# Kernel optimization log

Measured on AMD Instinct MI355X. Metric: run time of the kernel, lower is better.

## Reference

```python
import jax, jax.numpy as jnp
import numpy as np

N = 8192          # rays
S = 128           # steps per ray (cfg.n_steps_fixed)
POS_BANDS = 10    # positional-encoding bands for positions
VD_BANDS = 4      # bands for view directions (default in _encode_viewdir)
EARLY_STOP_T = 1e-4


def pos_enc(x, num_bands):
    """[..., 3] -> [..., 3 + 2*3*num_bands], interleaved [x, sin(f*x), cos(f*x), ...]."""
    parts = [x]
    for i in range(num_bands):  # small fixed loop over frequency bands
        f = jnp.asarray(2.0 ** i, dtype=x.dtype)
        parts.append(jnp.sin(f * x))
        parts.append(jnp.cos(f * x))
    return jnp.concatenate(parts, axis=-1)


def setup_inputs() -> dict:
    key = jax.random.key(0)
    ks = jax.random.split(key, 10)
    orig = 0.1 * jax.random.normal(ks[0], (N, 3), jnp.float32)
    dirs = jax.random.normal(ks[1], (N, 3), jnp.float32)
    dirs = dirs / (jnp.linalg.norm(dirs, axis=-1, keepdims=True) + 1e-8)
    tmin = 0.5 + 0.5 * jax.random.uniform(ks[2], (N,), jnp.float32)
    tmax = tmin + 1.0 + jax.random.uniform(ks[3], (N,), jnp.float32)
    d_enc = 3 + 2 * 3 * POS_BANDS          # 63
    d_vd = 3 + 2 * 3 * VD_BANDS            # 27
    hid, feat = 64, 15
    W1 = jax.random.normal(ks[4], (d_enc, hid), jnp.float32) / np.sqrt(d_enc)
    b1 = jnp.zeros((hid,), jnp.float32)
    W2 = jax.random.normal(ks[5], (hid, 1 + feat), jnp.float32) / np.sqrt(hid)
    b2 = jnp.zeros((1 + feat,), jnp.float32)
    V1 = jax.random.normal(ks[6], (feat + d_vd, hid), jnp.float32) / np.sqrt(feat + d_vd)
    c1 = jnp.zeros((hid,), jnp.float32)
    V2 = jax.random.normal(ks[7], (hid, 3), jnp.float32) / np.sqrt(hid)
    c2 = jnp.zeros((3,), jnp.float32)
    return {"orig": orig, "dirs": dirs, "tmin": tmin, "tmax": tmax,
            "W1": W1, "b1": b1, "W2": W2, "b2": b2,
            "V1": V1, "c1": c1, "V2": V2, "c2": c2}


def reference(orig, dirs, tmin, tmax, W1, b1, W2, b2, V1, c1, V2, c2):
    # --- fixed-step sampling ---
    t_uniform = jnp.linspace(0.0, 1.0, S, dtype=jnp.float32)          # [S]
    t = tmin[:, None] + t_uniform[None, :] * (tmax - tmin)[:, None]   # [N, S]
    dt = jnp.mean(tmax - tmin) / S                                    # scalar step size

    # --- positions and encoder ---
    pos = orig[:, None, :] + dirs[:, None, :] * t[..., None]          # [N, S, 3]
    enc = pos_enc(pos, POS_BANDS)                                     # [N, S, 63]

    # --- field MLP: sigma + rgb features ---
    h = jax.nn.relu(enc @ W1 + b1)                                    # [N, S, 64]
    out = h @ W2 + b2                                                 # [N, S, 16]
    sigma = jax.nn.relu(out[..., 0])                                  # [N, S]
    rgb_feat = out[..., 1:]                                           # [N, S, 15]

    # --- rgb head with view-direction PE ---
    vd = dirs / (jnp.linalg.norm(dirs, axis=-1, keepdims=True) + 1e-8)
    vd_enc = pos_enc(vd, VD_BANDS)                                    # [N, 27]
    vd_enc = jnp.broadcast_to(vd_enc[:, None, :], (rgb_feat.shape[0], S, vd_enc.shape[-1]))
    rgb_in = jnp.concatenate([rgb_feat, vd_enc], axis=-1)             # [N, S, 42]
    rgb_steps = jax.nn.sigmoid(jax.nn.relu(rgb_in @ V1 + c1) @ V2 + c2)  # [N, S, 3]

    # --- alpha compositing with early stop (dense-masked equivalent) ---
    alpha = 1.0 - jnp.exp(-sigma * dt)                                # [N, S]
    one_minus = 1.0 - alpha
    T_excl = jnp.concatenate(
        [jnp.ones_like(alpha[:, :1]), jnp.cumprod(one_minus, axis=1)[:, :-1]], axis=1
    )                                                                 # transmittance before each step
    active = T_excl > EARLY_STOP_T                                    # ray still marching
    weights = T_excl * alpha * active                                 # [N, S]
    rgb_out = jnp.sum(weights[..., None] * rgb_steps, axis=1)         # [N, 3]
    T_out = jnp.prod(jnp.where(active, one_minus, 1.0), axis=1)       # final transmittance at stop
    return rgb_out, T_out
```

## Files before the change

### kernel.cpp

```cpp
#include <hip/hip_runtime.h>
#include <hip/hip_bf16.h>

#define NRAYS 8192
#define SAMP  128
#define DVD   27
#define NFEAT 15

typedef float  f32x4  __attribute__((ext_vector_type(4)));
typedef short  short8 __attribute__((ext_vector_type(8)));
typedef unsigned int u32x2 __attribute__((ext_vector_type(2)));

static __device__ __forceinline__ void stbf(short* p, float x) {
    union { unsigned u; struct { short lo, hi; } s; } v;
    v.u = __float_as_uint(x) + 0x8000u;
    *p = v.s.hi;
}
static __device__ __forceinline__ float bf2f(short s) {
    return __uint_as_float(((unsigned)(unsigned short)s) << 16);
}
static __device__ __forceinline__ unsigned pk2bf(float lo, float hi) {
    unsigned r;
    asm("v_cvt_pk_bf16_f32 %0, %1, %2" : "=v"(r) : "v"(lo), "v"(hi));
    return r;
}
static __device__ __forceinline__ float sin_fast(float x) {
    float r = x * 0.15915494309189535f;
    r = r - floorf(r);
    return __builtin_amdgcn_sinf(r);
}
static __device__ __forceinline__ float cos_fast(float x) {
    float r = x * 0.15915494309189535f;
    r = r - floorf(r);
    return __builtin_amdgcn_cosf(r);
}

#define SMEM_BYTES 32208

__global__ void __launch_bounds__(256)
march_kernel(const float* __restrict__ orig,
             const float* __restrict__ dirs,
             const float* __restrict__ tmin,
             const float* __restrict__ tmax,
             const float* __restrict__ W1,
             const float* __restrict__ b1,
             const float* __restrict__ W2,
             const float* __restrict__ b2,
             const float* __restrict__ V1,
             const float* __restrict__ c1,
             const float* __restrict__ V2,
             const float* __restrict__ c2,
             float* __restrict__ out) {
    __shared__ __align__(16) char smem[SMEM_BYTES];
    short* const sW1t = (short*)(smem);
    short* const sW2t = (short*)(smem + 9216);
    short* const sV1t = (short*)(smem + 11520);
    short* const sV2t = (short*)(smem + 15616);
    short* const sEa  = (short*)(smem);
    short* const sGa  = (short*)(smem + 18432);
    float* const sOm  = (float*)(smem + 26624);
    short* const sRgb = (short*)(smem + 28672);
    float* const sVde = (float*)(smem + 31744);
    float* const sRed = (float*)(smem + 32192);

    const int tid  = threadIdx.x;
    const int lane = tid & 63;
    const int wave = tid >> 6;
    const int ray  = blockIdx.x * 4 + wave;

    {
        const float4* tm0 = (const float4*)tmin;
        const float4* tm1 = (const float4*)tmax;
        float s = 0.0f;
        #pragma unroll
        for (int it = 0; it < 8; it++) {
            const int i = tid + it * 256;
            const float4 a = tm1[i], b = tm0[i];
            s += (a.x - b.x) + (a.y - b.y) + (a.z - b.z) + (a.w - b.w);
        }
        #pragma unroll
        for (int off = 32; off > 0; off >>= 1)
            s += __shfl_xor(s, off, 64);
        if (lane == 0) sRed[wave] = s;
    }

    for (int i = tid; i < 63 * 64; i += 256) {
        const int k = i >> 6, n = i & 63;
        const int nk = (k < 3) ? (60 + k) : (k - 3);
        stbf(&sW1t[n * 72 + nk], W1[i]);
    }
    for (int i = tid; i < 64; i += 256)
        stbf(&sW1t[i * 72 + 63], b1[i]);
    for (int i = tid; i < 64 * 16; i += 256) {
        const int k = i >> 4, n = i & 15;
        stbf(&sW2t[n * 72 + k], W2[i]);
    }
    for (int i = tid; i < 15 * 64; i += 256) {
        const int k = i >> 6, n = i & 63;
        stbf(&sV1t[n * 32 + k], V1[i]);
    }
    for (int i = tid; i < 64; i += 256)
        stbf(&sV1t[i * 32 + 15], c1[i]);
    for (int i = tid; i < 64 * 16; i += 256) {
        const int n = i >> 4, k = 16 + (i & 15);
        sV1t[n * 32 + k] = 0;
    }
    for (int i = tid; i < 192; i += 256) {
        const int k = i / 3, n = i - 3 * k;
        stbf(&sV2t[n * 72 + k], V2[i]);
    }

    const float ox = orig[ray * 3 + 0];
    const float oy = orig[ray * 3 + 1];
    const float oz = orig[ray * 3 + 2];
    const float dx = dirs[ray * 3 + 0];
    const float dy = dirs[ray * 3 + 1];
    const float dz = dirs[ray * 3 + 2];
    const float t0v = tmin[ray];
    const float trange = tmax[ray] - t0v;

    {
        const float nrm = sqrtf(dx * dx + dy * dy + dz * dz);
        const float inv = 1.0f / (nrm + 1e-8f);
        const float vx = dx * inv, vy = dy * inv, vz = dz * inv;
        if (lane < DVD) {
            float val;
            if (lane < 3) {
                val = (lane == 0) ? vx : ((lane == 1) ? vy : vz);
            } else {
                const int q = lane - 3;
                const int b = q / 6;
                const int r = q - 6 * b;
                const bool isSin = (r < 3);
                const int d = isSin ? r : (r - 3);
                const float comp = (d == 0) ? vx : ((d == 1) ? vy : vz);
                const float a = (float)(1 << b) * comp;
                val = isSin ? sin_fast(a) : cos_fast(a);
            }
            sVde[wave * 28 + lane] = val;
        }
    }
    __syncthreads();

    const float dtv = (sRed[0] + sRed[1] + sRed[2] + sRed[3]) *
                      (1.0f / ((float)NRAYS * (float)SAMP));

    const int nfr  = lane & 15;
    const int quad = lane >> 4;

    short8 w1f[4][2], w2f[2], v1f[4], v2f[2];
    #pragma unroll
    for (int nt = 0; nt < 4; nt++)
        #pragma unroll
        for (int kt = 0; kt < 2; kt++)
            w1f[nt][kt] = *(const short8*)&sW1t[(4 * nfr + nt) * 72 + quad * 8 + kt * 32];
    #pragma unroll
    for (int kt = 0; kt < 2; kt++)
        w2f[kt] = *(const short8*)&sW2t[nfr * 72 + quad * 8 + kt * 32];
    #pragma unroll
    for (int nt = 0; nt < 4; nt++)
        v1f[nt] = *(const short8*)&sV1t[(4 * nfr + nt) * 32 + quad * 8];
    #pragma unroll
    for (int kt = 0; kt < 2; kt++) {
        if (nfr < 3)
            v2f[kt] = *(const short8*)&sV2t[nfr * 72 + quad * 8 + kt * 32];
        else
            v2f[kt] = (short8){0, 0, 0, 0, 0, 0, 0, 0};
    }

    const float bb2 = b2[nfr];
    const float bc2 = (nfr < 3) ? c2[nfr] : 0.0f;

    float gv[4] = {0.0f, 0.0f, 0.0f, 0.0f};
    #pragma unroll 1
    for (int q = 0; q < DVD; q++) {
        const float e = sVde[wave * 28 + q];
        const f32x4 vv = *(const f32x4*)&V1[(NFEAT + q) * 64 + 4 * nfr];
        gv[0] += e * vv.x; gv[1] += e * vv.y;
        gv[2] += e * vv.z; gv[3] += e * vv.w;
    }
    __syncthreads();

    short* const myE = sEa + wave * (32 * 72);
    short* const myG = sGa + wave * (32 * 32);
    {
        int* gz = (int*)myG;
        for (int i = lane; i < 32 * 16; i += 64) gz[i] = 0;
    }
    if (lane < 32) myG[lane * 32 + 15] = (short)0x3F80;

    const int sl   = lane >> 1;
    const int half = lane & 1;
    const float fmul = half ? 5.0929581789406507f
                            : 0.15915494309189535f;

    #pragma unroll 1
    for (int qq = 0; qq < 4; qq++) {
        {
            const int s = qq * 32 + sl;
            const float t = t0v + (float)s * (1.0f / 127.0f) * trange;
            const float px = ox + dx * t, py = oy + dy * t, pz = oz + dz * t;
            unsigned* Edw = (unsigned*)&myE[sl * 72];
            unsigned* Eh  = Edw + 15 * half;
            float rx = px * fmul; rx -= floorf(rx);
            float ry = py * fmul; ry -= floorf(ry);
            float rz = pz * fmul; rz -= floorf(rz);
            float sx = __builtin_amdgcn_sinf(rx), cx = __builtin_amdgcn_cosf(rx);
            float sy = __builtin_amdgcn_sinf(ry), cy = __builtin_amdgcn_cosf(ry);
            float sz = __builtin_amdgcn_sinf(rz), cz = __builtin_amdgcn_cosf(rz);
            #pragma unroll
            for (int j = 0; j < 5; j++) {
                Eh[3 * j + 0] = pk2bf(sx, sy);
                Eh[3 * j + 1] = pk2bf(sz, cx);
                Eh[3 * j + 2] = pk2bf(cy, cz);
                if (j < 4) {
                    const float tx = sx + sx, ty = sy + sy, tz = sz + sz;
                    const float nsx = tx * cx, nsy = ty * cy, nsz = tz * cz;
                    cx = __builtin_fmaf(-tx, sx, 1.0f);
                    cy = __builtin_fmaf(-ty, sy, 1.0f);
                    cz = __builtin_fmaf(-tz, sz, 1.0f);
                    sx = nsx; sy = nsy; sz = nsz;
                }
            }
            if (half == 0) {
                u32x2 xyz;
                xyz.x = pk2bf(px, py);
                xyz.y = pk2bf(pz, 1.0f);
                *(u32x2*)(Edw + 30) = xyz;
            }
        }
        f32x4 acc1[2][4];
        #pragma unroll
        for (int mt = 0; mt < 2; mt++)
            #pragma unroll
            for (int nt = 0; nt < 4; nt++)
                acc1[mt][nt] = (f32x4){0.0f, 0.0f, 0.0f, 0.0f};
        {
            short8 af[2][2];
            #pragma unroll
            for (int mt = 0; mt < 2; mt++)
                #pragma unroll
                for (int kt = 0; kt < 2; kt++)
                    af[mt][kt] = *(const short8*)&myE[(nfr + 16 * mt) * 72 + quad * 8 + kt * 32];
            #pragma unroll
            for (int mt = 0; mt < 2; mt++)
                #pragma unroll
                for (int nt = 0; nt < 4; nt++)
                    #pragma unroll
                    for (int kt = 0; kt < 2; kt++)
                        acc1[mt][nt] = __builtin_amdgcn_mfma_f32_16x16x32_bf16(
                            af[mt][kt], w1f[nt][kt], acc1[mt][nt], 0, 0, 0);
        }
        #pragma unroll
        for (int mt = 0; mt < 2; mt++)
            #pragma unroll
            for (int r = 0; r < 4; r++) {
                const int m = 4 * quad + r + 16 * mt;
                u32x2 hp;
                hp.x = pk2bf(fmaxf(acc1[mt][0][r], 0.0f),
                             fmaxf(acc1[mt][1][r], 0.0f));
                hp.y = pk2bf(fmaxf(acc1[mt][2][r], 0.0f),
                             fmaxf(acc1[mt][3][r], 0.0f));
                *(u32x2*)&myE[m * 72 + 4 * nfr] = hp;
            }
        f32x4 acc2[2];
        acc2[0] = (f32x4){0.0f, 0.0f, 0.0f, 0.0f};
        acc2[1] = (f32x4){0.0f, 0.0f, 0.0f, 0.0f};
        {
            short8 ah[2][2];
            #pragma unroll
            for (int mt = 0; mt < 2; mt++)
                #pragma unroll
                for (int kt = 0; kt < 2; kt++)
                    ah[mt][kt] = *(const short8*)&myE[(nfr + 16 * mt) * 72 + quad * 8 + kt * 32];
            #pragma unroll
            for (int mt = 0; mt < 2; mt++)
                #pragma unroll
                for (int kt = 0; kt < 2; kt++)
                    acc2[mt] = __builtin_amdgcn_mfma_f32_16x16x32_bf16(
                        ah[mt][kt], w2f[kt], acc2[mt], 0, 0, 0);
        }
        if (nfr == 0) {
            #pragma unroll
            for (int mt = 0; mt < 2; mt++)
                #pragma unroll
                for (int r = 0; r < 4; r++) {
                    const int m = 4 * quad + r + 16 * mt;
                    const float sg = fmaxf(acc2[mt][r] + bb2, 0.0f);
                    sOm[wave * 128 + qq * 32 + m] = __expf(-sg * dtv);
                }
        } else {
            #pragma unroll
            for (int mt = 0; mt < 2; mt++)
                #pragma unroll
                for (int r = 0; r < 4; r++) {
                    const int m = 4 * quad + r + 16 * mt;
                    stbf(&myG[m * 32 + (nfr - 1)], acc2[mt][r] + bb2);
                }
        }
        f32x4 acc3[2][4];
        #pragma unroll
        for (int mt = 0; mt < 2; mt++)
            #pragma unroll
            for (int nt = 0; nt < 4; nt++)
                acc3[mt][nt] = (f32x4){0.0f, 0.0f, 0.0f, 0.0f};
        {
            short8 ag[2];
            #pragma unroll
            for (int mt = 0; mt < 2; mt++)
                ag[mt] = *(const short8*)&myG[(nfr + 16 * mt) * 32 + quad * 8];
            #pragma unroll
            for (int mt = 0; mt < 2; mt++)
                #pragma unroll
                for (int nt = 0; nt < 4; nt++)
                    acc3[mt][nt] = __builtin_amdgcn_mfma_f32_16x16x32_bf16(
                        ag[mt], v1f[nt], acc3[mt][nt], 0, 0, 0);
        }
        #pragma unroll
        for (int mt = 0; mt < 2; mt++)
            #pragma unroll
            for (int r = 0; r < 4; r++) {
                const int m = 4 * quad + r + 16 * mt;
                u32x2 gp;
                gp.x = pk2bf(fmaxf(acc3[mt][0][r] + gv[0], 0.0f),
                             fmaxf(acc3[mt][1][r] + gv[1], 0.0f));
                gp.y = pk2bf(fmaxf(acc3[mt][2][r] + gv[2], 0.0f),
                             fmaxf(acc3[mt][3][r] + gv[3], 0.0f));
                *(u32x2*)&myE[m * 72 + 4 * nfr] = gp;
            }
        f32x4 acc4[2];
        acc4[0] = (f32x4){0.0f, 0.0f, 0.0f, 0.0f};
        acc4[1] = (f32x4){0.0f, 0.0f, 0.0f, 0.0f};
        {
            short8 agg[2][2];
            #pragma unroll
            for (int mt = 0; mt < 2; mt++)
                #pragma unroll
                for (int kt = 0; kt < 2; kt++)
                    agg[mt][kt] = *(const short8*)&myE[(nfr + 16 * mt) * 72 + quad * 8 + kt * 32];
            #pragma unroll
            for (int mt = 0; mt < 2; mt++)
                #pragma unroll
                for (int kt = 0; kt < 2; kt++)
                    acc4[mt] = __builtin_amdgcn_mfma_f32_16x16x32_bf16(
                        agg[mt][kt], v2f[kt], acc4[mt], 0, 0, 0);
        }
        if (nfr < 3) {
            #pragma unroll
            for (int mt = 0; mt < 2; mt++)
                #pragma unroll
                for (int r = 0; r < 4; r++) {
                    const int m = 4 * quad + r + 16 * mt;
                    const float val = acc4[mt][r] + bc2;
                    stbf(&sRgb[wave * 384 + (qq * 32 + m) * 3 + nfr],
                         1.0f / (1.0f + __expf(-val)));
                }
        }
    }

    const float om0 = sOm[wave * 128 + 2 * lane];
    const float om1 = sOm[wave * 128 + 2 * lane + 1];
    const float al0 = 1.0f - om0;
    const float al1 = 1.0f - om1;

    float inc = om0 * om1;
    #pragma unroll
    for (int off = 1; off < 64; off <<= 1) {
        const float q = __shfl_up(inc, off, 64);
        if (lane >= off) inc *= q;
    }
    float Texc = __shfl_up(inc, 1, 64);
    if (lane == 0) Texc = 1.0f;

    const float T0 = Texc;
    const float T1 = Texc * om0;
    const float a0 = (T0 > 1e-4f) ? 1.0f : 0.0f;
    const float a1 = (T1 > 1e-4f) ? 1.0f : 0.0f;
    const float w0 = T0 * al0 * a0;
    const float w1 = T1 * al1 * a1;

    float cr = w0 * bf2f(sRgb[wave * 384 + (2 * lane) * 3 + 0]) +
               w1 * bf2f(sRgb[wave * 384 + (2 * lane + 1) * 3 + 0]);
    float cg = w0 * bf2f(sRgb[wave * 384 + (2 * lane) * 3 + 1]) +
               w1 * bf2f(sRgb[wave * 384 + (2 * lane + 1) * 3 + 1]);
    float cb = w0 * bf2f(sRgb[wave * 384 + (2 * lane) * 3 + 2]) +
               w1 * bf2f(sRgb[wave * 384 + (2 * lane + 1) * 3 + 2]);
    float tp = (a0 > 0.0f ? om0 : 1.0f) * (a1 > 0.0f ? om1 : 1.0f);

    #pragma unroll
    for (int off = 32; off > 0; off >>= 1) {
        cr += __shfl_xor(cr, off, 64);
        cg += __shfl_xor(cg, off, 64);
        cb += __shfl_xor(cb, off, 64);
        tp *= __shfl_xor(tp, off, 64);
    }

    if (lane == 0) {
        out[ray * 3 + 0] = cr;
        out[ray * 3 + 1] = cg;
        out[ray * 3 + 2] = cb;
        out[NRAYS * 3 + ray] = tp;
    }
}

extern "C" void kernel_launch(void* const* d_in, const int* in_sizes, int n_in,
                              void* d_out, int out_size, void* d_ws, size_t ws_size,
                              hipStream_t stream) {
    const float* orig = (const float*)d_in[0];
    const float* dirs = (const float*)d_in[1];
    const float* tmin = (const float*)d_in[2];
    const float* tmax = (const float*)d_in[3];
    const float* W1   = (const float*)d_in[4];
    const float* b1   = (const float*)d_in[5];
    const float* W2   = (const float*)d_in[6];
    const float* b2   = (const float*)d_in[7];
    const float* V1   = (const float*)d_in[8];
    const float* c1   = (const float*)d_in[9];
    const float* V2   = (const float*)d_in[10];
    const float* c2   = (const float*)d_in[11];

    march_kernel<<<NRAYS / 4, 256, 0, stream>>>(orig, dirs, tmin, tmax,
                                                W1, b1, W2, b2, V1, c1, V2, c2,
                                                (float*)d_out);
}
```

Baseline: 133.2 us.

## Fold W2-feature and V1 layers into combined matrix built by a prep kernel

Adds a prep kernel that converts all weights to bf16 once, lays them out as an image in workspace, and multiplies the feature columns of W2 with the matching rows of V1 into one 64x64 matrix, with the bias folded into gvc. The march kernel no longer rounds the feature layer to bf16 in LDS and runs a third GEMM on it. Instead it applies the combined matrix directly to the hidden activations and copies the prebuilt image into LDS with vector loads instead of converting weights per block. Encoding rows are also written with 16-byte stores in a new column order. This trades a small second launch and more MFMAs in stage two for removing the per-block weight conversion and the intermediate LDS round trip.

```diff
diff --git a/kernel.cpp b/kernel.cpp
--- a/kernel.cpp
+++ b/kernel.cpp
@@ -9,6 +9,14 @@
 typedef float  f32x4  __attribute__((ext_vector_type(4)));
 typedef short  short8 __attribute__((ext_vector_type(8)));
 typedef unsigned int u32x2 __attribute__((ext_vector_type(2)));
+typedef unsigned int u32x4 __attribute__((ext_vector_type(4)));
+
+#define IMG_W1   0
+#define IMG_C    4608
+#define IMG_W2S  9216
+#define IMG_V2   10368
+#define IMG_SHORTS 10584
+#define GVC_OFF  21168
 
 static __device__ __forceinline__ void stbf(short* p, float x) {
     union { unsigned u; struct { short lo, hi; } s; } v;
@@ -34,33 +42,83 @@
     return __builtin_amdgcn_cosf(r);
 }
 
-#define SMEM_BYTES 32208
+static __device__ __forceinline__ int kmap(int r) {
+    if (r == 0) return 30;
+    if (r == 1) return 31;
+    if (r == 2) return 62;
+    const int q = r - 3, i = q / 6, c = q - 6 * i;
+    return (i < 5 ? 6 * i : 32 + 6 * (i - 5)) + c;
+}
+
+__global__ void __launch_bounds__(256)
+prep_kernel(const float* __restrict__ W1, const float* __restrict__ b1,
+            const float* __restrict__ W2, const float* __restrict__ b2,
+            const float* __restrict__ V1, const float* __restrict__ c1,
+            const float* __restrict__ V2, short* __restrict__ img,
+            float* __restrict__ gvc) {
+    const int g = blockIdx.x * 256 + threadIdx.x;
+    if (g < 4032) {
+        const int r = g >> 6, n = g & 63;
+        stbf(&img[IMG_W1 + n * 72 + kmap(r)], W1[g]);
+    } else if (g < 4096) {
+        const int n = g - 4032;
+        stbf(&img[IMG_W1 + n * 72 + 63], b1[n]);
+    } else {
+        const int i = g - 4096;
+        const int k = i >> 6, n = i & 63;
+        float a = 0.0f;
+        #pragma unroll
+        for (int j = 0; j < 15; j++) a += W2[k * 16 + 1 + j] * V1[j * 64 + n];
+        stbf(&img[IMG_C + n * 72 + k], a);
+    }
+    if (g < 64) {
+        stbf(&img[IMG_W2S + g], W2[g * 16]);
+    } else if (g < 256) {
+        const int i = g - 64, k = i / 3, n = i - 3 * k;
+        stbf(&img[IMG_V2 + n * 72 + k], V2[i]);
+    } else if (g < 320) {
+        const int n = g - 256;
+        float a = c1[n];
+        #pragma unroll
+        for (int j = 0; j < 15; j++) a += b2[1 + j] * V1[j * 64 + n];
+        gvc[n] = a;
+    } else if (g < 1496) {
+        const int z = g - 320, row = z >> 3, c = z & 7;
+        int base;
+        if (row < 64)       base = IMG_W1  + row * 72;
+        else if (row < 128) base = IMG_C   + (row - 64) * 72;
+        else if (row < 144) base = IMG_W2S + (row - 128) * 72;
+        else                base = IMG_V2  + (row - 144) * 72;
+        img[base + 64 + c] = 0;
+    } else if (g < 2456) {
+        const int z = g - 1496, n = 1 + (z >> 6), k = z & 63;
+        img[IMG_W2S + n * 72 + k] = 0;
+    }
+}
+
+#define SMEM_BYTES 26768
 
 __global__ void __launch_bounds__(256)
 march_kernel(const float* __restrict__ orig,
              const float* __restrict__ dirs,
              const float* __restrict__ tmin,
              const float* __restrict__ tmax,
-             const float* __restrict__ W1,
-             const float* __restrict__ b1,
-             const float* __restrict__ W2,
              const float* __restrict__ b2,
+             const float* __restrict__ c2,
              const float* __restrict__ V1,
-             const float* __restrict__ c1,
-             const float* __restrict__ V2,
-             const float* __restrict__ c2,
+             const short* __restrict__ img,
+             const float* __restrict__ gvc,
              float* __restrict__ out) {
     __shared__ __align__(16) char smem[SMEM_BYTES];
     short* const sW1t = (short*)(smem);
-    short* const sW2t = (short*)(smem + 9216);
-    short* const sV1t = (short*)(smem + 11520);
-    short* const sV2t = (short*)(smem + 15616);
+    short* const sCt  = (short*)(smem + 9216);
+    short* const sW2s = (short*)(smem + 18432);
+    short* const sV2t = (short*)(smem + 20736);
     short* const sEa  = (short*)(smem);
-    short* const sGa  = (short*)(smem + 18432);
-    float* const sOm  = (float*)(smem + 26624);
-    short* const sRgb = (short*)(smem + 28672);
-    float* const sVde = (float*)(smem + 31744);
-    float* const sRed = (float*)(smem + 32192);
+    float* const sOm  = (float*)(smem + 21184);
+    short* const sRgb = (short*)(smem + 23232);
+    float* const sVde = (float*)(smem + 26304);
+    float* const sRed = (float*)(smem + 26752);
 
     const int tid  = threadIdx.x;
     const int lane = tid & 63;
@@ -83,30 +141,14 @@
         if (lane == 0) sRed[wave] = s;
     }
 
-    for (int i = tid; i < 63 * 64; i += 256) {
-        const int k = i >> 6, n = i & 63;
-        const int nk = (k < 3) ? (60 + k) : (k - 3);
-        stbf(&sW1t[n * 72 + nk], W1[i]);
-    }
-    for (int i = tid; i < 64; i += 256)
-        stbf(&sW1t[i * 72 + 63], b1[i]);
-    for (int i = tid; i < 64 * 16; i += 256) {
-        const int k = i >> 4, n = i & 15;
-        stbf(&sW2t[n * 72 + k], W2[i]);
-    }
-    for (int i = tid; i < 15 * 64; i += 256) {
-        const int k = i >> 6, n = i & 63;
-        stbf(&sV1t[n * 32 + k], V1[i]);
-    }
-    for (int i = tid; i < 64; i += 256)
-        stbf(&sV1t[i * 32 + 15], c1[i]);
-    for (int i = tid; i < 64 * 16; i += 256) {
-        const int n = i >> 4, k = 16 + (i & 15);
-        sV1t[n * 32 + k] = 0;
-    }
-    for (int i = tid; i < 192; i += 256) {
-        const int k = i / 3, n = i - 3 * k;
-        stbf(&sV2t[n * 72 + k], V2[i]);
+    {
+        const u32x4* src = (const u32x4*)img;
+        u32x4* dst = (u32x4*)smem;
+        #pragma unroll
+        for (int it = 0; it < 6; it++) {
+            const int i = tid + it * 256;
+            if (i < IMG_SHORTS / 8) dst[i] = src[i];
+        }
     }
 
     const float ox = orig[ray * 3 + 0];
@@ -147,18 +189,17 @@
     const int nfr  = lane & 15;
     const int quad = lane >> 4;
 
-    short8 w1f[4][2], w2f[2], v1f[4], v2f[2];
+    short8 w1f[4][2], combf[4][2], w2sf[2], v2f[2];
     #pragma unroll
     for (int nt = 0; nt < 4; nt++)
         #pragma unroll
-        for (int kt = 0; kt < 2; kt++)
-            w1f[nt][kt] = *(const short8*)&sW1t[(4 * nfr + nt) * 72 + quad * 8 + kt * 32];
+        for (int kt = 0; kt < 2; kt++) {
+            w1f[nt][kt]   = *(const short8*)&sW1t[(4 * nfr + nt) * 72 + quad * 8 + kt * 32];
+            combf[nt][kt] = *(const short8*)&sCt [(4 * nfr + nt) * 72 + quad * 8 + kt * 32];
+        }
     #pragma unroll
     for (int kt = 0; kt < 2; kt++)
-        w2f[kt] = *(const short8*)&sW2t[nfr * 72 + quad * 8 + kt * 32];
-    #pragma unroll
-    for (int nt = 0; nt < 4; nt++)
-        v1f[nt] = *(const short8*)&sV1t[(4 * nfr + nt) * 32 + quad * 8];
+        w2sf[kt] = *(const short8*)&sW2s[nfr * 72 + quad * 8 + kt * 32];
     #pragma unroll
     for (int kt = 0; kt < 2; kt++) {
         if (nfr < 3)
@@ -167,11 +208,15 @@
             v2f[kt] = (short8){0, 0, 0, 0, 0, 0, 0, 0};
     }
 
-    const float bb2 = b2[nfr];
+    const float bb2 = b2[0];
     const float bc2 = (nfr < 3) ? c2[nfr] : 0.0f;
 
-    float gv[4] = {0.0f, 0.0f, 0.0f, 0.0f};
-    #pragma unroll 1
+    float gv[4];
+    {
+        const f32x4 g0 = *(const f32x4*)&gvc[4 * nfr];
+        gv[0] = g0.x; gv[1] = g0.y; gv[2] = g0.z; gv[3] = g0.w;
+    }
+    #pragma unroll 9
     for (int q = 0; q < DVD; q++) {
         const float e = sVde[wave * 28 + q];
         const f32x4 vv = *(const f32x4*)&V1[(NFEAT + q) * 64 + 4 * nfr];
@@ -181,12 +226,6 @@
     __syncthreads();
 
     short* const myE = sEa + wave * (32 * 72);
-    short* const myG = sGa + wave * (32 * 32);
-    {
-        int* gz = (int*)myG;
-        for (int i = lane; i < 32 * 16; i += 64) gz[i] = 0;
-    }
-    if (lane < 32) myG[lane * 32 + 15] = (short)0x3F80;
 
     const int sl   = lane >> 1;
     const int half = lane & 1;
@@ -199,19 +238,18 @@
             const int s = qq * 32 + sl;
             const float t = t0v + (float)s * (1.0f / 127.0f) * trange;
             const float px = ox + dx * t, py = oy + dy * t, pz = oz + dz * t;
-            unsigned* Edw = (unsigned*)&myE[sl * 72];
-            unsigned* Eh  = Edw + 15 * half;
             float rx = px * fmul; rx -= floorf(rx);
             float ry = py * fmul; ry -= floorf(ry);
             float rz = pz * fmul; rz -= floorf(rz);
             float sx = __builtin_amdgcn_sinf(rx), cx = __builtin_amdgcn_cosf(rx);
             float sy = __builtin_amdgcn_sinf(ry), cy = __builtin_amdgcn_cosf(ry);
             float sz = __builtin_amdgcn_sinf(rz), cz = __builtin_amdgcn_cosf(rz);
+            unsigned e[16] __attribute__((aligned(16)));
             #pragma unroll
             for (int j = 0; j < 5; j++) {
-                Eh[3 * j + 0] = pk2bf(sx, sy);
-                Eh[3 * j + 1] = pk2bf(sz, cx);
-                Eh[3 * j + 2] = pk2bf(cy, cz);
+                e[3 * j + 0] = pk2bf(sx, sy);
+                e[3 * j + 1] = pk2bf(sz, cx);
+                e[3 * j + 2] = pk2bf(cy, cz);
                 if (j < 4) {
                     const float tx = sx + sx, ty = sy + sy, tz = sz + sz;
                     const float nsx = tx * cx, nsy = ty * cy, nsz = tz * cz;
@@ -221,12 +259,12 @@
                     sx = nsx; sy = nsy; sz = nsz;
                 }
             }
-            if (half == 0) {
-                u32x2 xyz;
-                xyz.x = pk2bf(px, py);
-                xyz.y = pk2bf(pz, 1.0f);
-                *(u32x2*)(Edw + 30) = xyz;
-            }
+            e[15] = half ? pk2bf(pz, 1.0f) : pk2bf(px, py);
+            u32x4* dst = (u32x4*)((unsigned*)&myE[sl * 72] + 16 * half);
+            dst[0] = *(const u32x4*)&e[0];
+            dst[1] = *(const u32x4*)&e[4];
+            dst[2] = *(const u32x4*)&e[8];
+            dst[3] = *(const u32x4*)&e[12];
         }
         f32x4 acc1[2][4];
         #pragma unroll
@@ -263,8 +301,14 @@
                 *(u32x2*)&myE[m * 72 + 4 * nfr] = hp;
             }
         f32x4 acc2[2];
+        f32x4 acc3[2][4];
         acc2[0] = (f32x4){0.0f, 0.0f, 0.0f, 0.0f};
         acc2[1] = (f32x4){0.0f, 0.0f, 0.0f, 0.0f};
+        #pragma unroll
+        for (int mt = 0; mt < 2; mt++)
+            #pragma unroll
+            for (int nt = 0; nt < 4; nt++)
+                acc3[mt][nt] = (f32x4){0.0f, 0.0f, 0.0f, 0.0f};
         {
             short8 ah[2][2];
             #pragma unroll
@@ -277,7 +321,15 @@
                 #pragma unroll
                 for (int kt = 0; kt < 2; kt++)
                     acc2[mt] = __builtin_amdgcn_mfma_f32_16x16x32_bf16(
-                        ah[mt][kt], w2f[kt], acc2[mt], 0, 0, 0);
+                        ah[mt][kt], w2sf[kt], acc2[mt], 0, 0, 0);
+            #pragma unroll
+            for (int mt = 0; mt < 2; mt++)
+                #pragma unroll
+                for (int nt = 0; nt < 4; nt++)
+                    #pragma unroll
+                    for (int kt = 0; kt < 2; kt++)
+                        acc3[mt][nt] = __builtin_amdgcn_mfma_f32_16x16x32_bf16(
+                            ah[mt][kt], combf[nt][kt], acc3[mt][nt], 0, 0, 0);
         }
         if (nfr == 0) {
             #pragma unroll
@@ -288,32 +340,6 @@
                     const float sg = fmaxf(acc2[mt][r] + bb2, 0.0f);
                     sOm[wave * 128 + qq * 32 + m] = __expf(-sg * dtv);
                 }
-        } else {
-            #pragma unroll
-            for (int mt = 0; mt < 2; mt++)
-                #pragma unroll
-                for (int r = 0; r < 4; r++) {
-                    const int m = 4 * quad + r + 16 * mt;
-                    stbf(&myG[m * 32 + (nfr - 1)], acc2[mt][r] + bb2);
-                }
-        }
-        f32x4 acc3[2][4];
-        #pragma unroll
-        for (int mt = 0; mt < 2; mt++)
-            #pragma unroll
-            for (int nt = 0; nt < 4; nt++)
-                acc3[mt][nt] = (f32x4){0.0f, 0.0f, 0.0f, 0.0f};
-        {
-            short8 ag[2];
-            #pragma unroll
-            for (int mt = 0; mt < 2; mt++)
-                ag[mt] = *(const short8*)&myG[(nfr + 16 * mt) * 32 + quad * 8];
-            #pragma unroll
-            for (int mt = 0; mt < 2; mt++)
-                #pragma unroll
-                for (int nt = 0; nt < 4; nt++)
-                    acc3[mt][nt] = __builtin_amdgcn_mfma_f32_16x16x32_bf16(
-                        ag[mt], v1f[nt], acc3[mt][nt], 0, 0, 0);
         }
         #pragma unroll
         for (int mt = 0; mt < 2; mt++)
@@ -418,7 +444,11 @@
     const float* V2   = (const float*)d_in[10];
     const float* c2   = (const float*)d_in[11];
 
+    short* img = (short*)d_ws;
+    float* gvc = (float*)((char*)d_ws + GVC_OFF);
+
+    prep_kernel<<<32, 256, 0, stream>>>(W1, b1, W2, b2, V1, c1, V2, img, gvc);
     march_kernel<<<NRAYS / 4, 256, 0, stream>>>(orig, dirs, tmin, tmax,
-                                                W1, b1, W2, b2, V1, c1, V2, c2,
+                                                b2, c2, V1, img, gvc,
                                                 (float*)d_out);
 }
```

After: 142.4 us. 1.07x slower.
